# Optimization experiments

Measured on AMD Instinct MI355X. Metric: run time of the kernel, lower is better.

## Reference

```python
import jax, jax.numpy as jnp
import numpy as np
from jax.scipy.special import logsumexp

B, T, D, L = 64, 512, 1024, 16


def setup_inputs() -> dict:
    key = jax.random.key(0)
    ks = jax.random.split(key, 6)
    x = jax.random.normal(ks[0], (B, T, D), dtype=jnp.float32)
    mask = jnp.ones((B, T), dtype=bool)
    labels = jax.random.randint(ks[1], (B, T), 0, L)
    W = jax.random.normal(ks[2], (D, L), dtype=jnp.float32) * (1.0 / np.sqrt(D))
    b = jnp.zeros((L,), dtype=jnp.float32)
    transitions = jax.random.normal(ks[3], (L, L), dtype=jnp.float32) * 0.1
    start_trans = jax.random.normal(ks[4], (L,), dtype=jnp.float32) * 0.1
    end_trans = jax.random.normal(ks[5], (L,), dtype=jnp.float32) * 0.1
    return {"x": x, "mask": mask, "labels": labels, "W": W, "b": b,
            "transitions": transitions, "start_trans": start_trans, "end_trans": end_trans}


def _crf_loss(x, mask, labels, W, b, transitions, start_trans, end_trans):
    logits = jnp.einsum("btd,dl->btl", x, W) + b  # (B,T,L)
    maskf = mask.astype(logits.dtype)

    # ---- log partition via forward algorithm (scan over time) ----
    logits_t = jnp.swapaxes(logits, 0, 1)  # (T,B,L)
    mask_t = jnp.swapaxes(mask, 0, 1)      # (T,B)
    alpha0 = start_trans + logits_t[0]     # (B,L)

    def step(alpha, inp):
        emit, m = inp  # emit: (B,L), m: (B,)
        # transitions[i,j]: from tag i to tag j
        inner = alpha[:, :, None] + transitions[None, :, :] + emit[:, None, :]
        new = logsumexp(inner, axis=1)
        alpha = jnp.where(m[:, None], new, alpha)
        return alpha, None

    alpha, _ = jax.lax.scan(step, alpha0, (logits_t[1:], mask_t[1:]))
    log_z = logsumexp(alpha + end_trans, axis=-1)  # (B,)

    # ---- joint score of gold path ----
    emit = jnp.take_along_axis(logits, labels[..., None], axis=2)[..., 0]  # (B,T)
    emit_score = jnp.sum(emit * maskf, axis=1)
    trans = transitions[labels[:, :-1], labels[:, 1:]]  # (B,T-1)
    trans_score = jnp.sum(trans * maskf[:, 1:], axis=1)
    last_idx = jnp.sum(mask.astype(jnp.int32), axis=1) - 1  # (B,)
    last_tag = jnp.take_along_axis(labels, last_idx[:, None], axis=1)[:, 0]
    score = start_trans[labels[:, 0]] + emit_score + trans_score + end_trans[last_tag]

    log_likelihood = jnp.sum(score - log_z)
    return -log_likelihood  # loss


def reference(x, mask, labels, W, b, transitions, start_trans, end_trans):
    return _crf_loss(x, mask, labels, W, b, transitions, start_trans, end_trans)
```

## Files before the change

kernel.cpp:

```cpp
#include <hip/hip_runtime.h>

#define B_ 64
#define T_ 512
#define D_ 1024
#define L_ 16

typedef __attribute__((ext_vector_type(8))) short short8;
typedef __attribute__((ext_vector_type(4))) float f32x4;
typedef __attribute__((ext_vector_type(4))) float fvec4;

__device__ __forceinline__ unsigned bfpack(float lo, float hi) {
    unsigned a = __float_as_uint(lo), b = __float_as_uint(hi);
    a = (a + 0x7FFFu + ((a >> 16) & 1u)) >> 16;
    b = (b + 0x7FFFu + ((b >> 16) & 1u)) & 0xFFFF0000u;
    return a | b;
}

__global__ __launch_bounds__(256) void crf_gemm_scan(
        const float* __restrict__ x, const float* __restrict__ W,
        const float* __restrict__ bias, const float* __restrict__ trans,
        const float* __restrict__ startt, const int* __restrict__ labels,
        float* __restrict__ Pmat, float* __restrict__ SsA,
        float* __restrict__ scA, float* __restrict__ outz) {
    constexpr int LDU = 1040;
    constexpr int EMS = 20;
    __shared__ __align__(16) unsigned short xs[16 * LDU];
    __shared__ float part[4][16][16];
    __shared__ __align__(16) float em[16 * EMS];
    __shared__ __align__(16) float etr[16 * EMS];
    const int tid  = threadIdx.x;
    const int l    = tid & 63;
    const int kq   = tid >> 6;
    const int quad = l >> 4;
    const int m    = l & 15;
    const int bk   = blockIdx.x;
    const int r0   = bk * 16;
    if (bk == 0 && tid == 0) outz[0] = 0.f;

    const fvec4* gx = reinterpret_cast<const fvec4*>(x + (size_t)r0 * D_);
    fvec4 stg[16];
#pragma unroll
    for (int i = 0; i < 16; ++i) {
        asm volatile("global_load_dwordx4 %0, %1, off sc0 sc1 nt"
                     : "=&v"(stg[i])
                     : "v"(gx + i * 256 + tid)
                     : "memory");
    }

    uint4 wf[8];
#pragma unroll
    for (int c = 0; c < 8; ++c) {
        const int k0 = kq * 256 + c * 32 + quad * 8;
        unsigned u0 = bfpack(W[(size_t)(k0 + 0) * L_ + m], W[(size_t)(k0 + 1) * L_ + m]);
        unsigned u1 = bfpack(W[(size_t)(k0 + 2) * L_ + m], W[(size_t)(k0 + 3) * L_ + m]);
        unsigned u2 = bfpack(W[(size_t)(k0 + 4) * L_ + m], W[(size_t)(k0 + 5) * L_ + m]);
        unsigned u3 = bfpack(W[(size_t)(k0 + 6) * L_ + m], W[(size_t)(k0 + 7) * L_ + m]);
        wf[c] = make_uint4(u0, u1, u2, u3);
    }

    etr[(tid >> 4) * EMS + (tid & 15)] = __expf(trans[tid]);

    asm volatile("s_waitcnt vmcnt(0)" ::: "memory");
    __builtin_amdgcn_sched_barrier(0);

#pragma unroll
    for (int i = 0; i < 16; ++i) {
        unsigned u0 = bfpack(stg[i].x, stg[i].y);
        unsigned u1 = bfpack(stg[i].z, stg[i].w);
        *reinterpret_cast<uint2*>(&xs[i * LDU + 4 * tid]) = make_uint2(u0, u1);
    }
    __syncthreads();

    f32x4 acc = {0.f, 0.f, 0.f, 0.f};
#pragma unroll
    for (int c = 0; c < 8; ++c) {
        const unsigned short* xr = &xs[m * LDU + (kq * 8 + c) * 32 + quad * 8];
        union { uint2 v[2]; short8 s; } a;
        a.v[0] = *reinterpret_cast<const uint2*>(xr);
        a.v[1] = *reinterpret_cast<const uint2*>(xr + 4);
        union { uint4 u; short8 s; } b;
        b.u = wf[c];
        acc = __builtin_amdgcn_mfma_f32_16x16x32_bf16(a.s, b.s, acc, 0, 0, 0);
    }
#pragma unroll
    for (int r = 0; r < 4; ++r) part[kq][quad * 4 + r][m] = acc[r];
    __syncthreads();

    {
        const int row = tid >> 4, col = tid & 15;
        float s = part[0][row][col] + part[1][row][col] + part[2][row][col] +
                  part[3][row][col] + bias[col];
        em[row * EMS + col] = s;
    }
    __syncthreads();

    const int w = tid >> 6;
    const int batch = bk >> 5;
    const int tt0   = (bk & 31) * 16;

    if (w == 0) {
        const int i  = l & 15;
        const int jq = l >> 4;
        float p0, p1, p2, p3, S = 0.f;
        if (tt0 == 0) {
            float a0 = startt[i] + em[i];
            float m0 = a0;
#pragma unroll
            for (int ww = 1; ww < 16; ww <<= 1) m0 = fmaxf(m0, __shfl_xor(m0, ww));
            float e0 = __expf(a0 - m0);
            p0 = (i == (jq << 2) + 0) ? e0 : 0.f;
            p1 = (i == (jq << 2) + 1) ? e0 : 0.f;
            p2 = (i == (jq << 2) + 2) ? e0 : 0.f;
            p3 = (i == (jq << 2) + 3) ? e0 : 0.f;
            S = m0;
        } else {
            p0 = (i == (jq << 2) + 0) ? 1.f : 0.f;
            p1 = (i == (jq << 2) + 1) ? 1.f : 0.f;
            p2 = (i == (jq << 2) + 2) ? 1.f : 0.f;
            p3 = (i == (jq << 2) + 3) ? 1.f : 0.f;
        }
        const int s0 = (tt0 == 0) ? 1 : 0;
        for (int s = s0; s < 16; ++s) {
            float4 emv = *reinterpret_cast<const float4*>(&em[s * EMS + (jq << 2)]);
            float mx = fmaxf(fmaxf(emv.x, emv.y), fmaxf(emv.z, emv.w));
            mx = fmaxf(mx, __shfl_xor(mx, 16));
            mx = fmaxf(mx, __shfl_xor(mx, 32));
            S += mx;
            float qx = __expf(emv.x - mx), qy = __expf(emv.y - mx);
            float qz = __expf(emv.z - mx), qw = __expf(emv.w - mx);
            float r[4][4];
            r[0][0] = p0; r[0][1] = p1; r[0][2] = p2; r[0][3] = p3;
#pragma unroll
            for (int g = 1; g < 4; ++g) {
                r[g][0] = __shfl_xor(p0, g << 4);
                r[g][1] = __shfl_xor(p1, g << 4);
                r[g][2] = __shfl_xor(p2, g << 4);
                r[g][3] = __shfl_xor(p3, g << 4);
            }
            float ax = 0.f, ay = 0.f, az = 0.f, aw = 0.f;
#pragma unroll
            for (int g = 0; g < 4; ++g)
#pragma unroll
                for (int t = 0; t < 4; ++t) {
                    float4 e = *reinterpret_cast<const float4*>(
                        &etr[(((jq ^ g) << 2) + t) * EMS + (jq << 2)]);
                    ax = fmaf(r[g][t], e.x, ax);
                    ay = fmaf(r[g][t], e.y, ay);
                    az = fmaf(r[g][t], e.z, az);
                    aw = fmaf(r[g][t], e.w, aw);
                }
            ax *= qx; ay *= qy; az *= qz; aw *= qw;
            if ((s & 3) == 3) {
                float mm = fmaxf(fmaxf(ax, ay), fmaxf(az, aw));
#pragma unroll
                for (int ww = 1; ww < 64; ww <<= 1) mm = fmaxf(mm, __shfl_xor(mm, ww));
                unsigned eb = (__float_as_uint(mm) >> 23) & 0xFFu;
                float scl = __uint_as_float((254u - eb) << 23);
                ax *= scl; ay *= scl; az *= scl; aw *= scl;
                S += ((int)eb - 127) * 0.69314718056f;
            }
            p0 = ax; p1 = ay; p2 = az; p3 = aw;
        }
        *reinterpret_cast<float4*>(&Pmat[(size_t)bk * 256 + i * 16 + (jq << 2)]) =
            make_float4(p0, p1, p2, p3);
        if (l == 0) SsA[bk] = S;
    } else if (w == 1) {
        float sc = 0.f;
        if (l < 16) {
            const int t = tt0 + l;
            const int base = batch * T_;
            int lt = labels[base + t];
            sc = em[l * EMS + lt];
            if (t >= 1) sc += trans[labels[base + t - 1] * L_ + lt];
        }
#pragma unroll
        for (int ww = 1; ww < 16; ww <<= 1) sc += __shfl_xor(sc, ww);
        if (l == 0) scA[bk] = sc;
    }
}

__global__ __launch_bounds__(64) void crf_combine(
        const float* __restrict__ Pmat, const float* __restrict__ SsA,
        const float* __restrict__ scA, const int* __restrict__ labels,
        const float* __restrict__ startt, const float* __restrict__ endt,
        float* __restrict__ out) {
    const int b = blockIdx.x;
    const int l = threadIdx.x;
    const int j = l & 15;
    const int kq = l >> 4;
    float v = 1.f, S2 = 0.f;
    for (int c = 0; c < 32; ++c) {
        const float* rec = Pmat + (size_t)(b * 32 + c) * 256;
        float cur[4];
#pragma unroll
        for (int t = 0; t < 4; ++t) cur[t] = rec[((kq << 2) + t) * 16 + j];
        float pt = 0.f;
#pragma unroll
        for (int t = 0; t < 4; ++t)
            pt = fmaf(__shfl(v, (l & 48) + (kq << 2) + t), cur[t], pt);
        pt += __shfl_xor(pt, 16);
        pt += __shfl_xor(pt, 32);
        S2 += SsA[b * 32 + c];
        if ((c & 3) == 3) {
            float m = pt;
#pragma unroll
            for (int ww = 1; ww < 16; ww <<= 1) m = fmaxf(m, __shfl_xor(m, ww));
            unsigned eb = (__float_as_uint(m) >> 23) & 0xFFu;
            pt *= __uint_as_float((254u - eb) << 23);
            S2 += ((int)eb - 127) * 0.69314718056f;
        }
        v = pt;
    }
    float term = v * __expf(endt[j]);
#pragma unroll
    for (int ww = 1; ww < 16; ww <<= 1) term += __shfl_xor(term, ww);
    float logz = S2 + __logf(term);
    float sc = (l < 32) ? scA[b * 32 + l] : 0.f;
#pragma unroll
    for (int ww = 1; ww < 64; ww <<= 1) sc += __shfl_xor(sc, ww);
    if (l == 0) {
        sc += startt[labels[b * T_]] + endt[labels[b * T_ + T_ - 1]];
        atomicAdd(out, logz - sc);
    }
}

__global__ __launch_bounds__(256) void crf_gemm(const float* __restrict__ x,
                                                const float* __restrict__ W,
                                                const float* __restrict__ bias,
                                                float* __restrict__ logits,
                                                float* __restrict__ outz) {
    constexpr int LDU = 1040;
    __shared__ __align__(16) unsigned short xs[16 * LDU];
    __shared__ float part[4][16][16];
    const int tid  = threadIdx.x;
    const int l    = tid & 63;
    const int kq   = tid >> 6;
    const int quad = l >> 4;
    const int m    = l & 15;
    const int r0   = blockIdx.x * 16;
    if (blockIdx.x == 0 && tid == 0) outz[0] = 0.f;
    const fvec4* gx = reinterpret_cast<const fvec4*>(x + (size_t)r0 * D_);
    fvec4 stg[16];
#pragma unroll
    for (int i = 0; i < 16; ++i) {
        asm volatile("global_load_dwordx4 %0, %1, off sc0 sc1 nt"
                     : "=&v"(stg[i]) : "v"(gx + i * 256 + tid) : "memory");
    }
    uint4 wf[8];
#pragma unroll
    for (int c = 0; c < 8; ++c) {
        const int k0 = kq * 256 + c * 32 + quad * 8;
        unsigned u0 = bfpack(W[(size_t)(k0 + 0) * L_ + m], W[(size_t)(k0 + 1) * L_ + m]);
        unsigned u1 = bfpack(W[(size_t)(k0 + 2) * L_ + m], W[(size_t)(k0 + 3) * L_ + m]);
        unsigned u2 = bfpack(W[(size_t)(k0 + 4) * L_ + m], W[(size_t)(k0 + 5) * L_ + m]);
        unsigned u3 = bfpack(W[(size_t)(k0 + 6) * L_ + m], W[(size_t)(k0 + 7) * L_ + m]);
        wf[c] = make_uint4(u0, u1, u2, u3);
    }
    asm volatile("s_waitcnt vmcnt(0)" ::: "memory");
    __builtin_amdgcn_sched_barrier(0);
#pragma unroll
    for (int i = 0; i < 16; ++i) {
        unsigned u0 = bfpack(stg[i].x, stg[i].y);
        unsigned u1 = bfpack(stg[i].z, stg[i].w);
        *reinterpret_cast<uint2*>(&xs[i * LDU + 4 * tid]) = make_uint2(u0, u1);
    }
    __syncthreads();
    f32x4 acc = {0.f, 0.f, 0.f, 0.f};
#pragma unroll
    for (int c = 0; c < 8; ++c) {
        const unsigned short* xr = &xs[m * LDU + (kq * 8 + c) * 32 + quad * 8];
        union { uint2 v[2]; short8 s; } a;
        a.v[0] = *reinterpret_cast<const uint2*>(xr);
        a.v[1] = *reinterpret_cast<const uint2*>(xr + 4);
        union { uint4 u; short8 s; } b;
        b.u = wf[c];
        acc = __builtin_amdgcn_mfma_f32_16x16x32_bf16(a.s, b.s, acc, 0, 0, 0);
    }
#pragma unroll
    for (int r = 0; r < 4; ++r) part[kq][quad * 4 + r][m] = acc[r];
    __syncthreads();
    const int row = tid >> 4, col = tid & 15;
    float s = part[0][row][col] + part[1][row][col] + part[2][row][col] +
              part[3][row][col] + bias[col];
    logits[(size_t)(r0 + row) * L_ + col] = s;
}

__global__ __launch_bounds__(1024) void crf_rest(const float* __restrict__ logits,
                                                 const int* __restrict__ labels,
                                                 const float* __restrict__ trans,
                                                 const float* __restrict__ startt,
                                                 const float* __restrict__ endt,
                                                 float* __restrict__ out) {
    __shared__ float P[16][256];
    __shared__ float Ss[16];
    __shared__ float scoreP[16];
    const int b = blockIdx.x;
    const int tid = threadIdx.x;
    const int w = tid >> 6;
    const int l = tid & 63;
    const int i = l & 15;
    const int jq = l >> 4;
    const float* lg = logits + (size_t)b * (T_ * L_);
    float4 etp[4][4];
#pragma unroll
    for (int g = 0; g < 4; ++g)
#pragma unroll
        for (int t = 0; t < 4; ++t) {
            int k = ((jq ^ g) << 2) + t;
            float4 tv = *reinterpret_cast<const float4*>(&trans[k * L_ + (jq << 2)]);
            etp[g][t] = make_float4(__expf(tv.x), __expf(tv.y), __expf(tv.z), __expf(tv.w));
        }
    float p0 = (i == (jq << 2) + 0) ? 1.f : 0.f;
    float p1 = (i == (jq << 2) + 1) ? 1.f : 0.f;
    float p2 = (i == (jq << 2) + 2) ? 1.f : 0.f;
    float p3 = (i == (jq << 2) + 3) ? 1.f : 0.f;
    float S = 0.f;
    const int t0 = w * 32;
    float4 emn = *reinterpret_cast<const float4*>(&lg[(size_t)t0 * L_ + (jq << 2)]);
#pragma unroll 4
    for (int s = 0; s < 32; ++s) {
        float4 em = emn;
        if (s < 31)
            emn = *reinterpret_cast<const float4*>(&lg[(size_t)(t0 + s + 1) * L_ + (jq << 2)]);
        if (t0 + s >= 1) {
            float mx = fmaxf(fmaxf(em.x, em.y), fmaxf(em.z, em.w));
            mx = fmaxf(mx, __shfl_xor(mx, 16));
            mx = fmaxf(mx, __shfl_xor(mx, 32));
            S += mx;
            float qx = __expf(em.x - mx), qy = __expf(em.y - mx);
            float qz = __expf(em.z - mx), qw = __expf(em.w - mx);
            float r[4][4];
            r[0][0] = p0; r[0][1] = p1; r[0][2] = p2; r[0][3] = p3;
#pragma unroll
            for (int g = 1; g < 4; ++g) {
                r[g][0] = __shfl_xor(p0, g << 4);
                r[g][1] = __shfl_xor(p1, g << 4);
                r[g][2] = __shfl_xor(p2, g << 4);
                r[g][3] = __shfl_xor(p3, g << 4);
            }
            float ax = 0.f, ay = 0.f, az = 0.f, aw = 0.f;
#pragma unroll
            for (int g = 0; g < 4; ++g)
#pragma unroll
                for (int t = 0; t < 4; ++t) {
                    ax = fmaf(r[g][t], etp[g][t].x, ax);
                    ay = fmaf(r[g][t], etp[g][t].y, ay);
                    az = fmaf(r[g][t], etp[g][t].z, az);
                    aw = fmaf(r[g][t], etp[g][t].w, aw);
                }
            ax *= qx; ay *= qy; az *= qz; aw *= qw;
            if ((s & 3) == 3) {
                float m = fmaxf(fmaxf(ax, ay), fmaxf(az, aw));
#pragma unroll
                for (int ww = 1; ww < 64; ww <<= 1) m = fmaxf(m, __shfl_xor(m, ww));
                unsigned eb = (__float_as_uint(m) >> 23) & 0xFFu;
                float scl = __uint_as_float((254u - eb) << 23);
                ax *= scl; ay *= scl; az *= scl; aw *= scl;
                S += ((int)eb - 127) * 0.69314718056f;
            }
            p0 = ax; p1 = ay; p2 = az; p3 = aw;
        }
    }
    *reinterpret_cast<float4*>(&P[w][i * 16 + (jq << 2)]) = make_float4(p0, p1, p2, p3);
    if (l == 0) Ss[w] = S;
    float sc = 0.f;
    if (tid < T_) {
        int lt = labels[b * T_ + tid];
        sc = lg[tid * L_ + lt];
        if (tid >= 1) sc += trans[labels[b * T_ + tid - 1] * L_ + lt];
    }
#pragma unroll
    for (int ww = 1; ww < 64; ww <<= 1) sc += __shfl_xor(sc, ww);
    if (l == 0) scoreP[w] = sc;
    __syncthreads();
    if (w == 0) {
        const int j = l & 15;
        const int kq = l >> 4;
        float a0 = startt[j] + lg[j];
        float m0 = a0;
#pragma unroll
        for (int ww = 1; ww < 16; ww <<= 1) m0 = fmaxf(m0, __shfl_xor(m0, ww));
        float v = __expf(a0 - m0);
        float S2 = m0;
        for (int c = 0; c < 16; ++c) {
            float cur[4];
#pragma unroll
            for (int t = 0; t < 4; ++t) cur[t] = P[c][(kq * 4 + t) * 16 + j];
            float pt = 0.f;
#pragma unroll
            for (int t = 0; t < 4; ++t)
                pt = fmaf(__shfl(v, (l & 48) + kq * 4 + t), cur[t], pt);
            pt += __shfl_xor(pt, 16);
            pt += __shfl_xor(pt, 32);
            S2 += Ss[c];
            if ((c & 3) == 3) {
                float m = pt;
#pragma unroll
                for (int ww = 1; ww < 16; ww <<= 1) m = fmaxf(m, __shfl_xor(m, ww));
                unsigned eb = (__float_as_uint(m) >> 23) & 0xFFu;
                pt *= __uint_as_float((254u - eb) << 23);
                S2 += ((int)eb - 127) * 0.69314718056f;
            }
            v = pt;
        }
        float term = v * __expf(endt[j]);
#pragma unroll
        for (int ww = 1; ww < 16; ww <<= 1) term += __shfl_xor(term, ww);
        float logz = S2 + __logf(term);
        if (l == 0) {
            float score = startt[labels[b * T_]] + endt[labels[b * T_ + T_ - 1]];
#pragma unroll
            for (int q = 0; q < 16; ++q) score += scoreP[q];
            atomicAdd(out, logz - score);
        }
    }
}

extern "C" void kernel_launch(void* const* d_in, const int* in_sizes, int n_in,
                              void* d_out, int out_size, void* d_ws, size_t ws_size,
                              hipStream_t stream) {
    const float* x      = (const float*)d_in[0];
    const int*   labels = (const int*)d_in[2];
    const float* W      = (const float*)d_in[3];
    const float* bias   = (const float*)d_in[4];
    const float* trans  = (const float*)d_in[5];
    const float* startt = (const float*)d_in[6];
    const float* endt   = (const float*)d_in[7];
    float* out = (float*)d_out;

    const size_t NREC = 2048;
    const size_t need = (NREC * 256 + NREC + NREC) * 4;

    if (ws_size >= need) {
        float* Pmat = (float*)d_ws;
        float* SsA  = Pmat + NREC * 256;
        float* scA  = SsA + NREC;
        crf_gemm_scan<<<2048, 256, 0, stream>>>(x, W, bias, trans, startt,
                                                labels, Pmat, SsA, scA, out);
        crf_combine<<<B_, 64, 0, stream>>>(Pmat, SsA, scA, labels, startt,
                                           endt, out);
    } else {
        float* logits = (float*)d_ws;
        crf_gemm<<<2048, 256, 0, stream>>>(x, W, bias, logits, out);
        crf_rest<<<B_, 1024, 0, stream>>>(logits, labels, trans, startt, endt, out);
    }
}
```

Measured before the change: 217.2 us.

## Fuse per-batch combine into scan kernel via last-block atomic counter

```diff
diff --git a/kernel.cpp b/kernel.cpp
--- a/kernel.cpp
+++ b/kernel.cpp
@@ -16,12 +16,23 @@
     return a | b;
 }
 
+__device__ __forceinline__ void store_f32_sc(float* p, float v) {
+    asm volatile("global_store_dword %0, %1, off sc0 sc1" :: "v"(p), "v"(v) : "memory");
+}
+__device__ __forceinline__ float load_f32_sc(const float* p) {
+    float v;
+    asm volatile("global_load_dword %0, %1, off sc0 sc1\n\ts_waitcnt vmcnt(0)"
+                 : "=v"(v) : "v"(p) : "memory");
+    return v;
+}
+
 __global__ __launch_bounds__(256) void crf_gemm_scan(
         const float* __restrict__ x, const float* __restrict__ W,
         const float* __restrict__ bias, const float* __restrict__ trans,
-        const float* __restrict__ startt, const int* __restrict__ labels,
-        float* __restrict__ Pmat, float* __restrict__ SsA,
-        float* __restrict__ scA, float* __restrict__ outz) {
+        const float* __restrict__ startt, const float* __restrict__ endt,
+        const int* __restrict__ labels, float* __restrict__ Pmat,
+        float* __restrict__ SsA, float* __restrict__ scA,
+        unsigned* __restrict__ cnt, float* __restrict__ out) {
     constexpr int LDU = 1040;
     constexpr int EMS = 20;
     __shared__ __align__(16) unsigned short xs[16 * LDU];
@@ -35,16 +46,15 @@
     const int m    = l & 15;
     const int bk   = blockIdx.x;
     const int r0   = bk * 16;
-    if (bk == 0 && tid == 0) outz[0] = 0.f;
+    const int batch = bk >> 5;
+    const int tt0   = (bk & 31) * 16;
 
     const fvec4* gx = reinterpret_cast<const fvec4*>(x + (size_t)r0 * D_);
     fvec4 stg[16];
 #pragma unroll
     for (int i = 0; i < 16; ++i) {
         asm volatile("global_load_dwordx4 %0, %1, off sc0 sc1 nt"
-                     : "=&v"(stg[i])
-                     : "v"(gx + i * 256 + tid)
-                     : "memory");
+                     : "=&v"(stg[i]) : "v"(gx + i * 256 + tid) : "memory");
     }
 
     uint4 wf[8];
@@ -95,8 +105,6 @@
     __syncthreads();
 
     const int w = tid >> 6;
-    const int batch = bk >> 5;
-    const int tt0   = (bk & 31) * 16;
 
     if (w == 0) {
         const int i  = l & 15;
@@ -161,9 +169,11 @@
             }
             p0 = ax; p1 = ay; p2 = az; p3 = aw;
         }
-        *reinterpret_cast<float4*>(&Pmat[(size_t)bk * 256 + i * 16 + (jq << 2)]) =
-            make_float4(p0, p1, p2, p3);
-        if (l == 0) SsA[bk] = S;
+        fvec4 pv; pv.x = p0; pv.y = p1; pv.z = p2; pv.w = p3;
+        float* pdst = &Pmat[(size_t)bk * 256 + i * 16 + (jq << 2)];
+        asm volatile("global_store_dwordx4 %0, %1, off sc0 sc1"
+                     :: "v"(pdst), "v"(pv) : "memory");
+        if (l == 0) store_f32_sc(&SsA[bk], S);
     } else if (w == 1) {
         float sc = 0.f;
         if (l < 16) {
@@ -175,52 +185,93 @@
         }
 #pragma unroll
         for (int ww = 1; ww < 16; ww <<= 1) sc += __shfl_xor(sc, ww);
-        if (l == 0) scA[bk] = sc;
-    }
-}
-
-__global__ __launch_bounds__(64) void crf_combine(
-        const float* __restrict__ Pmat, const float* __restrict__ SsA,
-        const float* __restrict__ scA, const int* __restrict__ labels,
-        const float* __restrict__ startt, const float* __restrict__ endt,
-        float* __restrict__ out) {
-    const int b = blockIdx.x;
-    const int l = threadIdx.x;
-    const int j = l & 15;
-    const int kq = l >> 4;
-    float v = 1.f, S2 = 0.f;
-    for (int c = 0; c < 32; ++c) {
-        const float* rec = Pmat + (size_t)(b * 32 + c) * 256;
-        float cur[4];
-#pragma unroll
-        for (int t = 0; t < 4; ++t) cur[t] = rec[((kq << 2) + t) * 16 + j];
-        float pt = 0.f;
-#pragma unroll
-        for (int t = 0; t < 4; ++t)
-            pt = fmaf(__shfl(v, (l & 48) + (kq << 2) + t), cur[t], pt);
-        pt += __shfl_xor(pt, 16);
-        pt += __shfl_xor(pt, 32);
-        S2 += SsA[b * 32 + c];
-        if ((c & 3) == 3) {
-            float m = pt;
-#pragma unroll
-            for (int ww = 1; ww < 16; ww <<= 1) m = fmaxf(m, __shfl_xor(m, ww));
-            unsigned eb = (__float_as_uint(m) >> 23) & 0xFFu;
-            pt *= __uint_as_float((254u - eb) << 23);
-            S2 += ((int)eb - 127) * 0.69314718056f;
-        }
-        v = pt;
-    }
-    float term = v * __expf(endt[j]);
-#pragma unroll
-    for (int ww = 1; ww < 16; ww <<= 1) term += __shfl_xor(term, ww);
-    float logz = S2 + __logf(term);
-    float sc = (l < 32) ? scA[b * 32 + l] : 0.f;
-#pragma unroll
-    for (int ww = 1; ww < 64; ww <<= 1) sc += __shfl_xor(sc, ww);
-    if (l == 0) {
-        sc += startt[labels[b * T_]] + endt[labels[b * T_ + T_ - 1]];
-        atomicAdd(out, logz - sc);
+        if (l == 0) store_f32_sc(&scA[bk], sc);
+    }
+
+    asm volatile("s_waitcnt vmcnt(0)" ::: "memory");
+    __syncthreads();
+    int old = -1;
+    if (tid == 0) old = (int)atomicAdd(&cnt[batch], 1u);
+    if (w != 0) return;
+    old = __shfl(old, 0);
+    if (old != 31) return;
+
+    {
+        const int b32 = batch * 32;
+        const int j  = l & 15;
+        const int kt = l >> 4;
+        float ssv = 0.f, spv = 0.f;
+        if (l < 32) {
+            ssv = load_f32_sc(&SsA[b32 + l]);
+            spv = load_f32_sc(&scA[b32 + l]);
+        }
+        const float* base = Pmat + (size_t)b32 * 256;
+        float A0, A1, A2, A3, B0, B1, B2, B3;
+
+#define ISSUE(d0, d1, d2, d3, c)                                              \
+    do {                                                                      \
+        const float* rp_ = base + (size_t)(c) * 256 + (kt << 6) + j;          \
+        asm volatile("global_load_dword %0, %1, off sc0 sc1"                  \
+                     : "=v"(d0) : "v"(rp_) : "memory");                       \
+        asm volatile("global_load_dword %0, %1, off sc0 sc1"                  \
+                     : "=v"(d1) : "v"(rp_ + 16) : "memory");                  \
+        asm volatile("global_load_dword %0, %1, off sc0 sc1"                  \
+                     : "=v"(d2) : "v"(rp_ + 32) : "memory");                  \
+        asm volatile("global_load_dword %0, %1, off sc0 sc1"                  \
+                     : "=v"(d3) : "v"(rp_ + 48) : "memory");                  \
+    } while (0)
+
+#define CSTEP(d0, d1, d2, d3, c)                                              \
+    do {                                                                      \
+        float pt = 0.f;                                                       \
+        pt = fmaf(__shfl(v, (l & 48) + (kt << 2) + 0), d0, pt);               \
+        pt = fmaf(__shfl(v, (l & 48) + (kt << 2) + 1), d1, pt);               \
+        pt = fmaf(__shfl(v, (l & 48) + (kt << 2) + 2), d2, pt);               \
+        pt = fmaf(__shfl(v, (l & 48) + (kt << 2) + 3), d3, pt);               \
+        pt += __shfl_xor(pt, 16);                                             \
+        pt += __shfl_xor(pt, 32);                                             \
+        S2 += __shfl(ssv, c);                                                 \
+        if (((c) & 3) == 3) {                                                 \
+            float mm = pt;                                                    \
+            for (int ww = 1; ww < 16; ww <<= 1) mm = fmaxf(mm, __shfl_xor(mm, ww)); \
+            unsigned eb = (__float_as_uint(mm) >> 23) & 0xFFu;                \
+            pt *= __uint_as_float((254u - eb) << 23);                         \
+            S2 += ((int)eb - 127) * 0.69314718056f;                           \
+        }                                                                     \
+        v = pt;                                                               \
+    } while (0)
+
+        float v = 1.f, S2 = 0.f;
+        ISSUE(A0, A1, A2, A3, 0);
+#pragma unroll 1
+        for (int c = 0; c < 32; c += 2) {
+            ISSUE(B0, B1, B2, B3, c + 1);
+            asm volatile("s_waitcnt vmcnt(4)" ::: "memory");
+            __builtin_amdgcn_sched_barrier(0);
+            CSTEP(A0, A1, A2, A3, c);
+            if (c + 2 < 32) {
+                ISSUE(A0, A1, A2, A3, c + 2);
+                asm volatile("s_waitcnt vmcnt(4)" ::: "memory");
+            } else {
+                asm volatile("s_waitcnt vmcnt(0)" ::: "memory");
+            }
+            __builtin_amdgcn_sched_barrier(0);
+            CSTEP(B0, B1, B2, B3, c + 1);
+        }
+#undef ISSUE
+#undef CSTEP
+
+        float term = v * __expf(endt[j]);
+#pragma unroll
+        for (int ww = 1; ww < 16; ww <<= 1) term += __shfl_xor(term, ww);
+        float logz = S2 + __logf(term);
+        float sp = spv;
+#pragma unroll
+        for (int ww = 1; ww < 64; ww <<= 1) sp += __shfl_xor(sp, ww);
+        if (l == 0) {
+            sp += startt[labels[batch * T_]] + endt[labels[batch * T_ + T_ - 1]];
+            atomicAdd(out, logz - sp);
+        }
     }
 }
 
@@ -429,16 +480,17 @@
     float* out = (float*)d_out;
 
     const size_t NREC = 2048;
-    const size_t need = (NREC * 256 + NREC + NREC) * 4;
+    const size_t need = (NREC * 256 + NREC + NREC + B_) * 4;
 
     if (ws_size >= need) {
-        float* Pmat = (float*)d_ws;
-        float* SsA  = Pmat + NREC * 256;
-        float* scA  = SsA + NREC;
-        crf_gemm_scan<<<2048, 256, 0, stream>>>(x, W, bias, trans, startt,
-                                                labels, Pmat, SsA, scA, out);
-        crf_combine<<<B_, 64, 0, stream>>>(Pmat, SsA, scA, labels, startt,
-                                           endt, out);
+        float*    Pmat = (float*)d_ws;
+        float*    SsA  = Pmat + NREC * 256;
+        float*    scA  = SsA + NREC;
+        unsigned* cnt  = (unsigned*)(scA + NREC);
+        hipMemsetAsync(cnt, 0, B_ * 4, stream);
+        hipMemsetAsync(out, 0, 4, stream);
+        crf_gemm_scan<<<2048, 256, 0, stream>>>(x, W, bias, trans, startt, endt,
+                                                labels, Pmat, SsA, scA, cnt, out);
     } else {
         float* logits = (float*)d_ws;
         crf_gemm<<<2048, 256, 0, stream>>>(x, W, bias, logits, out);
```

Result: slower. 225.2 us (+3.7%).
